# Optimization experiments

Measured on AMD Instinct MI355X. Metric: run time of the kernel, lower is better.

## Reference

```python
import jax, jax.numpy as jnp
import numpy as np

B, C_IN, N_NODES = 128, 64, 1024
N_TRIPLES = 3 * (N_NODES - 1)  # node 0 is the shared zero vector


def _btc(x, idx, w, b):
    # x: [B, C, N]; idx: [B, 3M]; w: [O, C, 3]; b: [O]
    Bv, C, _ = x.shape
    T = idx.shape[1]
    g = jnp.take_along_axis(x, jnp.broadcast_to(idx[:, None, :], (Bv, C, T)), axis=2)
    g = g.reshape(Bv, C, T // 3, 3)  # stride-3 kernel-3 conv == per-triple contraction
    out = jnp.einsum('bcnk,ock->bon', g, w) + b[None, :, None]
    zero = jnp.zeros((Bv, out.shape[1], 1), dtype=out.dtype)
    return jnp.concatenate([zero, out], axis=2)  # re-prepend zero node -> [B, O, N]


def _tln(x):
    mean = jnp.mean(x, axis=(1, 2), keepdims=True)
    std = jnp.std(x, axis=(1, 2), ddof=1, keepdims=True)  # torch.std is unbiased
    return (x - mean) / (std + 1e-5)


def _tower(x, idx, p):
    x = jax.nn.leaky_relu(_tln(_btc(x, idx, p['w_conv1'], p['b_conv1'])), 0.01)
    x = jax.nn.leaky_relu(_tln(_btc(x, idx, p['w_conv2'], p['b_conv2'])), 0.01)
    x = _tln(_btc(x, idx, p['w_conv3'], p['b_conv3']))
    x = jnp.max(x, axis=2)  # DynamicPooling -> [B, 64]
    x = jax.nn.leaky_relu(x @ p['w_fc1'].T + p['b_fc1'], 0.01)
    return x @ p['w_fc2'].T + p['b_fc2']  # [B, 1]  (Dropout is identity at eval)


def setup_inputs() -> dict:
    key = jax.random.key(0)
    ks = jax.random.split(key, 12)
    s = 0.05
    return {
        'data1': jax.random.normal(ks[0], (B, C_IN, N_NODES), jnp.float32),
        'idx1': jax.random.randint(ks[1], (B, N_TRIPLES, 1), 0, N_NODES, dtype=jnp.int64)
                if jax.config.jax_enable_x64 else
                jax.random.randint(ks[1], (B, N_TRIPLES, 1), 0, N_NODES).astype(jnp.int32),
        'data2': jax.random.normal(ks[2], (B, C_IN, N_NODES), jnp.float32),
        'idx2': jax.random.randint(ks[3], (B, N_TRIPLES, 1), 0, N_NODES).astype(jnp.int32),
        'w_conv1': jax.random.normal(ks[4], (256, C_IN, 3), jnp.float32) * s,
        'b_conv1': jnp.zeros((256,), jnp.float32),
        'w_conv2': jax.random.normal(ks[5], (128, 256, 3), jnp.float32) * s,
        'b_conv2': jnp.zeros((128,), jnp.float32),
        'w_conv3': jax.random.normal(ks[6], (64, 128, 3), jnp.float32) * s,
        'b_conv3': jnp.zeros((64,), jnp.float32),
        'w_fc1': jax.random.normal(ks[7], (32, 64), jnp.float32) * s,
        'b_fc1': jnp.zeros((32,), jnp.float32),
        'w_fc2': jax.random.normal(ks[8], (1, 32), jnp.float32) * s,
        'b_fc2': jnp.zeros((1,), jnp.float32),
    }


def reference(data1, idx1, data2, idx2,
              w_conv1, b_conv1, w_conv2, b_conv2, w_conv3, b_conv3,
              w_fc1, b_fc1, w_fc2, b_fc2):
    p = dict(w_conv1=w_conv1, b_conv1=b_conv1, w_conv2=w_conv2, b_conv2=b_conv2,
             w_conv3=w_conv3, b_conv3=b_conv3, w_fc1=w_fc1, b_fc1=b_fc1,
             w_fc2=w_fc2, b_fc2=b_fc2)
    y1 = _tower(data1, idx1[..., 0], p)
    y2 = _tower(data2, idx2[..., 0], p)
    return jnp.squeeze(jax.nn.sigmoid(y1 - y2), axis=1)  # [B]
```

## Files before the change

### kernel.cpp

```cpp
#include <hip/hip_runtime.h>
#include <math.h>

typedef __attribute__((ext_vector_type(8))) short short8;
typedef __attribute__((ext_vector_type(4))) float f32x4;
typedef __attribute__((ext_vector_type(2))) float f32x2;

#define LRELU(x) ((x) > 0.0f ? (x) : 0.01f * (x))

__device__ __forceinline__ float bf2f(unsigned short h) {
    return __uint_as_float(((unsigned int)h) << 16);
}
__device__ __forceinline__ unsigned short f2bf(float f) {
    unsigned int u = __float_as_uint(f);
    return (unsigned short)((u + 0x7FFFu + ((u >> 16) & 1u)) >> 16);
}
__device__ __forceinline__ unsigned int pack_bf16_pair(float lo, float hi) {
    unsigned int ul = __float_as_uint(lo) + 0x8000u;
    unsigned int uh = __float_as_uint(hi) + 0x8000u;
    return (ul >> 16) | (uh & 0xFFFF0000u);
}
__device__ __forceinline__ float2 stats_from(const float* sums, int b, float count) {
    float s = sums[2 * b], q = sums[2 * b + 1];
    float mean = s / count;
    float var = (q - s * s / count) / (count - 1.0f);
    var = fmaxf(var, 0.0f);
    return make_float2(mean, 1.0f / (sqrtf(var) + 1e-5f));
}
__device__ __forceinline__ void atomicMaxF(float* a, float v) {
    if (v >= 0.0f) atomicMax((int*)a, __float_as_int(v));
    else           atomicMin((unsigned int*)a, __float_as_uint(v));
}
__device__ __forceinline__ unsigned int norm_pair(unsigned int u, float a, float c) {
    f32x2 v;
    v.x = __uint_as_float(u << 16);
    v.y = __uint_as_float(u & 0xFFFF0000u);
    v = v * a + c;
    f32x2 m = v * 0.01f;
    v = __builtin_elementwise_max(v, m);
    return pack_bf16_pair(v.x, v.y);
}
__device__ __forceinline__ uint4 norm8(uint4 v, float a, float c) {
    v.x = norm_pair(v.x, a, c); v.y = norm_pair(v.y, a, c);
    v.z = norm_pair(v.z, a, c); v.w = norm_pair(v.w, a, c);
    return v;
}
__device__ __forceinline__ unsigned int fp8x4_nact(unsigned int u, float a, float c) {
    f32x2 lo = __builtin_amdgcn_cvt_pk_f32_fp8(u, false);
    f32x2 hi = __builtin_amdgcn_cvt_pk_f32_fp8(u, true);
    lo = lo * a + c; hi = hi * a + c;
    f32x2 ml = lo * 0.01f, mh = hi * 0.01f;
    lo = __builtin_elementwise_max(lo, ml);
    hi = __builtin_elementwise_max(hi, mh);
    int r = __builtin_amdgcn_cvt_pk_fp8_f32(lo.x, lo.y, 0, false);
    r = __builtin_amdgcn_cvt_pk_fp8_f32(hi.x, hi.y, r, true);
    return (unsigned int)r;
}

template <int MT, int WM>
__device__ __forceinline__ void mfma_step(const unsigned short* wt, const unsigned short* gt,
                                          f32x4 (&acc)[MT][4],
                                          int wo, int wn, int quad, int l15, int blkid)
{
#pragma unroll
    for (int st = 0; st < 2; ++st) {
        short8 af[MT], bfv[4];
        const int qb = st * 4 + quad;
#pragma unroll
        for (int i = 0; i < MT; i++) {
            const int orow = wo * WM + i * 16 + l15;
            af[i] = *(const short8*)&wt[orow * 64 + ((qb ^ blkid) << 3)];
        }
#pragma unroll
        for (int t = 0; t < 4; t++) {
            const int nrow = wn * 64 + t * 16 + l15;
            bfv[t] = *(const short8*)&gt[nrow * 64 + ((qb ^ blkid) << 3)];
        }
#pragma unroll
        for (int i = 0; i < MT; i++)
#pragma unroll
            for (int t = 0; t < 4; t++)
                acc[i][t] = __builtin_amdgcn_mfma_f32_16x16x32_bf16(
                    af[i], bfv[t], acc[i][t], 0, 0, 0);
    }
}

__global__ void prep_weights(const float* __restrict__ w, unsigned short* __restrict__ wq,
                             int O, int Cin)
{
    const int K = 3 * Cin, total = O * K;
    for (int i = blockIdx.x * blockDim.x + threadIdx.x; i < total;
         i += gridDim.x * blockDim.x) {
        int o = i / K, kp = i - o * K;
        int j = kp / Cin, c = kp - j * Cin;
        wq[i] = f2bf(w[(o * Cin + c) * 3 + j]);
    }
}

__global__ void prep_weights_fp8(const float* __restrict__ w, unsigned char* __restrict__ wq,
                                 int O, int Cin)
{
    const int K = 3 * Cin, total = (O * K) >> 2;
    for (int i = blockIdx.x * blockDim.x + threadIdx.x; i < total;
         i += gridDim.x * blockDim.x) {
        const int e0 = i << 2;
        const int o = e0 / K, kp0 = e0 - o * K;
        float f0, f1, f2, f3;
        {
            int kp = kp0 + 0, j = kp / Cin, c = kp - j * Cin; f0 = w[(o * Cin + c) * 3 + j];
        }
        {
            int kp = kp0 + 1, j = kp / Cin, c = kp - j * Cin; f1 = w[(o * Cin + c) * 3 + j];
        }
        {
            int kp = kp0 + 2, j = kp / Cin, c = kp - j * Cin; f2 = w[(o * Cin + c) * 3 + j];
        }
        {
            int kp = kp0 + 3, j = kp / Cin, c = kp - j * Cin; f3 = w[(o * Cin + c) * 3 + j];
        }
        int r = __builtin_amdgcn_cvt_pk_fp8_f32(f0, f1, 0, false);
        r = __builtin_amdgcn_cvt_pk_fp8_f32(f2, f3, r, true);
        *(unsigned int*)&wq[e0] = (unsigned int)r;
    }
}

__global__ __launch_bounds__(256) void transpose_in(const float* __restrict__ inA,
                                                    const float* __restrict__ inB,
                                                    unsigned short* __restrict__ xT)
{
    const int b = blockIdx.y, n0 = blockIdx.x * 64;
    const float* in = (b >= 128 ? inB : inA) + ((size_t)(b & 127) * 64) * 1024;
    const int tid = threadIdx.x;
    __shared__ float tile[64][65];
    const int nn = tid & 63, cw = tid >> 6;
#pragma unroll
    for (int i = 0; i < 16; i++) {
        int c = i * 4 + cw;
        tile[c][nn] = in[(size_t)c * 1024 + n0 + nn];
    }
    __syncthreads();
    const int n = tid >> 2, cp = (tid & 3) * 16;
    unsigned int pk[8];
#pragma unroll
    for (int i = 0; i < 8; i++) {
        unsigned short lo = f2bf(tile[cp + 2 * i][n]);
        unsigned short hi = f2bf(tile[cp + 2 * i + 1][n]);
        pk[i] = (unsigned int)lo | ((unsigned int)hi << 16);
    }
    unsigned short* dst = xT + ((size_t)b * 1024 + n0 + n) * 64 + cp;
    uint4 v0 = {pk[0], pk[1], pk[2], pk[3]};
    uint4 v1 = {pk[4], pk[5], pk[6], pk[7]};
    *(uint4*)dst = v0;
    *(uint4*)(dst + 8) = v1;
}

__global__ __launch_bounds__(256) void norm_act_fp8(unsigned char* __restrict__ a,
                                                    const float* __restrict__ sums,
                                                    float count)
{
    const int b = blockIdx.y;
    float2 st = stats_from(sums, b, count);
    const float na = st.y, nc = -st.x * st.y;
    uint4* p = (uint4*)(a + ((size_t)b << 18));
    const int base = blockIdx.x * 256 + threadIdx.x;
#pragma unroll
    for (int it = 0; it < 4; ++it) {
        const int idx = base + it * 4096;
        uint4 v = p[idx];
        v.x = fp8x4_nact(v.x, na, nc);
        v.y = fp8x4_nact(v.y, na, nc);
        v.z = fp8x4_nact(v.z, na, nc);
        v.w = fp8x4_nact(v.w, na, nc);
        p[idx] = v;
    }
}

template <int BM, bool POOL, bool NORM, bool FP8IN, bool FP8OUT>
__global__ __launch_bounds__(256, 2) void conv_mfma(
    const void* __restrict__ xTv,
    const int* __restrict__ idxA,
    const int* __restrict__ idxB,
    const unsigned short* __restrict__ wq,
    const float* __restrict__ bias,
    void* __restrict__ out,
    float* __restrict__ sums,
    float* __restrict__ pmax,
    const float* __restrict__ normSums,
    float normCount, int Cin, int cinShift, int O, int K)
{
    constexpr int WM = BM / 2, MT = WM / 16;
    constexpr int NW = (BM == 128) ? 4 : 2;
    const int b   = blockIdx.x;
    const int o0  = blockIdx.y * BM;
    const int nt0 = blockIdx.z << 7;
    const int tid = threadIdx.x;
    const int lane = tid & 63, wave = tid >> 6;
    const int wo = wave & 1, wn = wave >> 1;
    const int quad = lane >> 4, l15 = lane & 15;
    const int blkid = lane & 7;

    __shared__ __align__(16) unsigned short wt[BM * 64];
    __shared__ __align__(16) unsigned short gt[128 * 64];

    f32x4 acc[MT][4];
#pragma unroll
    for (int i = 0; i < MT; i++)
#pragma unroll
        for (int t = 0; t < 4; t++) acc[i][t] = (f32x4){0.f, 0.f, 0.f, 0.f};

    const unsigned short* xTb16 = (const unsigned short*)xTv + (((size_t)b) << 10) * (size_t)Cin;
    const unsigned char*  xTb8  = (const unsigned char*)xTv  + (((size_t)b) << 10) * (size_t)Cin;
    const int* idxb = (b >= 128 ? idxB : idxA) + (size_t)(b & 127) * 3069;

    float na = 1.0f, nc = 0.0f;
    if (NORM) {
        float2 st = stats_from(normSums, b, normCount);
        na = st.y; nc = -st.x * st.y;
    }

    const int gr = tid >> 1, gh = tid & 1;
    int s0, s1, s2;
    {
        int n = nt0 + gr;
        int t0 = (n == 0) ? 0 : (n - 1);
        s0 = idxb[3 * t0]; s1 = idxb[3 * t0 + 1]; s2 = idxb[3 * t0 + 2];
    }
    const int wr   = (BM == 128) ? (tid >> 1) : (tid >> 2);
    const int wseg = (BM == 128) ? (tid & 1) : (tid & 3);
    const unsigned short* wrow = wq + (size_t)(o0 + wr) * K + wseg * (NW * 8);
    const int gswz = gr & 7, wswz = wr & 7;

    uint4 g0A, g1A, g2A, g3A, w0A, w1A, w2A, w3A;
    uint4 g0B, g1B, g2B, g3B, w0B, w1B, w2B, w3B;

#define LOADC(S, KC) {                                                           \
        const int k64_ = (KC) << 6;                                              \
        const int j_   = k64_ >> cinShift;                                       \
        const int c0_  = k64_ & (Cin - 1);                                       \
        const int src_ = (j_ == 0) ? s0 : ((j_ == 1) ? s1 : s2);                 \
        if (FP8IN) {                                                             \
            const uint4* gp_ = (const uint4*)(xTb8 + (size_t)src_ * Cin + c0_ + gh * 32); \
            g0##S = gp_[0]; g1##S = gp_[1];                                      \
        } else {                                                                 \
            const uint4* gp_ = (const uint4*)(xTb16 + (size_t)src_ * Cin + c0_ + gh * 32); \
            g0##S = gp_[0]; g1##S = gp_[1]; g2##S = gp_[2]; g3##S = gp_[3];      \
        }                                                                        \
        const uint4* wp_ = (const uint4*)(wrow + k64_);                          \
        w0##S = wp_[0]; w1##S = wp_[1];                                          \
        if (NW == 4) { w2##S = wp_[2]; w3##S = wp_[3]; }                         \
    }

#define STAGE(S) {                                                               \
        uint4 h0, h1, h2, h3;                                                    \
        h0 = g0##S; h1 = g1##S; h2 = g2##S; h3 = g3##S;                          \
        if (NORM) {                                                              \
            h0 = norm8(h0, na, nc); h1 = norm8(h1, na, nc);                      \
            h2 = norm8(h2, na, nc); h3 = norm8(h3, na, nc);                      \
        }                                                                        \
        *(uint4*)&gt[gr * 64 + (((gh << 2) | 0) ^ gswz) * 8] = h0;               \
        *(uint4*)&gt[gr * 64 + (((gh << 2) | 1) ^ gswz) * 8] = h1;               \
        *(uint4*)&gt[gr * 64 + (((gh << 2) | 2) ^ gswz) * 8] = h2;               \
        *(uint4*)&gt[gr * 64 + (((gh << 2) | 3) ^ gswz) * 8] = h3;               \
        *(uint4*)&wt[wr * 64 + ((wseg * NW + 0) ^ wswz) * 8] = w0##S;            \
        *(uint4*)&wt[wr * 64 + ((wseg * NW + 1) ^ wswz) * 8] = w1##S;            \
        if (NW == 4) {                                                           \
            *(uint4*)&wt[wr * 64 + ((wseg * NW + 2) ^ wswz) * 8] = w2##S;        \
            *(uint4*)&wt[wr * 64 + ((wseg * NW + 3) ^ wswz) * 8] = w3##S;        \
        }                                                                        \
    }

    const int nChunks = K >> 6;
    LOADC(A, 0);
    if (nChunks > 1) LOADC(B, 1);
    int kc = 0;
    for (; kc + 2 <= nChunks; kc += 2) {
        if (kc) __syncthreads();
        STAGE(A);
        if (kc + 2 < nChunks) LOADC(A, kc + 2);
        __syncthreads();
        mfma_step<MT, WM>(wt, gt, acc, wo, wn, quad, l15, blkid);
        __syncthreads();
        STAGE(B);
        if (kc + 3 < nChunks) LOADC(B, kc + 3);
        __syncthreads();
        mfma_step<MT, WM>(wt, gt, acc, wo, wn, quad, l15, blkid);
    }
    if (kc < nChunks) {
        __syncthreads();
        STAGE(A);
        __syncthreads();
        mfma_step<MT, WM>(wt, gt, acc, wo, wn, quad, l15, blkid);
    }
#undef LOADC
#undef STAGE

    float lsum = 0.f, lsq = 0.f;
#pragma unroll
    for (int i = 0; i < MT; i++) {
        const int ob = o0 + wo * WM + i * 16 + quad * 4;
        const float4 bv = *(const float4*)(bias + ob);
        float mx0 = -1e30f, mx1 = -1e30f, mx2 = -1e30f, mx3 = -1e30f;
#pragma unroll
        for (int t = 0; t < 4; t++) {
            const int n = nt0 + wn * 64 + t * 16 + l15;
            float v0 = acc[i][t][0] + bv.x;
            float v1 = acc[i][t][1] + bv.y;
            float v2 = acc[i][t][2] + bv.z;
            float v3 = acc[i][t][3] + bv.w;
            if (n == 0) { v0 = v1 = v2 = v3 = 0.f; }
            lsum += v0 + v1 + v2 + v3;
            lsq  += v0 * v0 + v1 * v1 + v2 * v2 + v3 * v3;
            if (POOL) {
                mx0 = fmaxf(mx0, v0); mx1 = fmaxf(mx1, v1);
                mx2 = fmaxf(mx2, v2); mx3 = fmaxf(mx3, v3);
            } else if (FP8OUT) {
                int r = __builtin_amdgcn_cvt_pk_fp8_f32(v0, v1, 0, false);
                r = __builtin_amdgcn_cvt_pk_fp8_f32(v2, v3, r, true);
                *(unsigned int*)&((unsigned char*)out)[((size_t)b * 1024 + n) * O + ob] =
                    (unsigned int)r;
            } else {
                uint2 pk;
                pk.x = pack_bf16_pair(v0, v1);
                pk.y = pack_bf16_pair(v2, v3);
                *(uint2*)&((unsigned short*)out)[((size_t)b * 1024 + n) * O + ob] = pk;
            }
        }
        if (POOL) {
#pragma unroll
            for (int off = 1; off < 16; off <<= 1) {
                mx0 = fmaxf(mx0, __shfl_xor(mx0, off));
                mx1 = fmaxf(mx1, __shfl_xor(mx1, off));
                mx2 = fmaxf(mx2, __shfl_xor(mx2, off));
                mx3 = fmaxf(mx3, __shfl_xor(mx3, off));
            }
            if (l15 == 0) {
                atomicMaxF(&pmax[(size_t)b * 64 + ob + 0], mx0);
                atomicMaxF(&pmax[(size_t)b * 64 + ob + 1], mx1);
                atomicMaxF(&pmax[(size_t)b * 64 + ob + 2], mx2);
                atomicMaxF(&pmax[(size_t)b * 64 + ob + 3], mx3);
            }
        }
    }
#pragma unroll
    for (int off = 32; off > 0; off >>= 1) {
        lsum += __shfl_down(lsum, off);
        lsq  += __shfl_down(lsq, off);
    }
    float* red = (float*)wt;
    if (lane == 0) { red[wave] = lsum; red[4 + wave] = lsq; }
    __syncthreads();
    if (tid == 0) {
        atomicAdd(&sums[2 * b + 0], red[0] + red[1] + red[2] + red[3]);
        atomicAdd(&sums[2 * b + 1], red[4] + red[5] + red[6] + red[7]);
    }
}

__global__ __launch_bounds__(256, 2) void conv2_fp8(
    const unsigned char* __restrict__ a1,
    const int* __restrict__ idxA,
    const int* __restrict__ idxB,
    const unsigned char* __restrict__ wq8,
    const float* __restrict__ bias,
    unsigned short* __restrict__ out,
    float* __restrict__ sums)
{
    const int b   = blockIdx.x;
    const int nt0 = blockIdx.z << 7;
    const int tid = threadIdx.x;
    const int lane = tid & 63, wave = tid >> 6;
    const int wo = wave & 1, wn = wave >> 1;
    const int quad = lane >> 4, l15 = lane & 15;
    const int blkid = lane & 7;

    __shared__ __align__(16) unsigned char wt8[128 * 128];
    __shared__ __align__(16) unsigned char gt8[128 * 128];

    f32x4 acc[4][4];
#pragma unroll
    for (int i = 0; i < 4; i++)
#pragma unroll
        for (int t = 0; t < 4; t++) acc[i][t] = (f32x4){0.f, 0.f, 0.f, 0.f};

    const unsigned char* xb = a1 + (((size_t)b) << 10) * 256;
    const int* idxb = (b >= 128 ? idxB : idxA) + (size_t)(b & 127) * 3069;

    const int gr = tid >> 1, gh = tid & 1;
    int si0, si1, si2;
    {
        int n = nt0 + gr;
        int t0 = (n == 0) ? 0 : (n - 1);
        si0 = idxb[3 * t0]; si1 = idxb[3 * t0 + 1]; si2 = idxb[3 * t0 + 2];
    }
    const unsigned char* wrow = wq8 + (size_t)gr * 768 + gh * 64;
    const int swz = gr & 7;

    uint4 g0A, g1A, g2A, g3A, w0A, w1A, w2A, w3A;
    uint4 g0B, g1B, g2B, g3B, w0B, w1B, w2B, w3B;

#define LOADC2(S, KC) {                                                          \
        const int j_  = (KC) >> 1;                                               \
        const int c0_ = ((KC) & 1) << 7;                                         \
        const int src_ = (j_ == 0) ? si0 : ((j_ == 1) ? si1 : si2);              \
        const uint4* gp_ = (const uint4*)(xb + (size_t)src_ * 256 + c0_ + gh * 64); \
        g0##S = gp_[0]; g1##S = gp_[1]; g2##S = gp_[2]; g3##S = gp_[3];          \
        const uint4* wp_ = (const uint4*)(wrow + (KC) * 128);                    \
        w0##S = wp_[0]; w1##S = wp_[1]; w2##S = wp_[2]; w3##S = wp_[3];          \
    }

#define STAGE2(S) {                                                              \
        *(uint4*)&gt8[gr * 128 + (((gh << 2) | 0) ^ swz) * 16] = g0##S;          \
        *(uint4*)&gt8[gr * 128 + (((gh << 2) | 1) ^ swz) * 16] = g1##S;          \
        *(uint4*)&gt8[gr * 128 + (((gh << 2) | 2) ^ swz) * 16] = g2##S;          \
        *(uint4*)&gt8[gr * 128 + (((gh << 2) | 3) ^ swz) * 16] = g3##S;          \
        *(uint4*)&wt8[gr * 128 + (((gh << 2) | 0) ^ swz) * 16] = w0##S;          \
        *(uint4*)&wt8[gr * 128 + (((gh << 2) | 1) ^ swz) * 16] = w1##S;          \
        *(uint4*)&wt8[gr * 128 + (((gh << 2) | 2) ^ swz) * 16] = w2##S;          \
        *(uint4*)&wt8[gr * 128 + (((gh << 2) | 3) ^ swz) * 16] = w3##S;          \
    }

#define MFMA_STEP2 {                                                             \
        _Pragma("unroll")                                                        \
        for (int st = 0; st < 4; ++st) {                                         \
            long af0, af1, af2, af3, bf0, bf1, bf2, bf3;                         \
            const int qb = st * 4 + quad;                                        \
            const int cg = qb >> 1, ch = (qb & 1) << 3;                          \
            {                                                                    \
                const int r0 = wo * 64 + 0 * 16 + l15;                           \
                af0 = *(const long*)&wt8[r0 * 128 + ((cg ^ blkid) << 4) + ch];   \
                const int r1 = wo * 64 + 1 * 16 + l15;                           \
                af1 = *(const long*)&wt8[r1 * 128 + ((cg ^ blkid) << 4) + ch];   \
                const int r2 = wo * 64 + 2 * 16 + l15;                           \
                af2 = *(const long*)&wt8[r2 * 128 + ((cg ^ blkid) << 4) + ch];   \
                const int r3 = wo * 64 + 3 * 16 + l15;                           \
                af3 = *(const long*)&wt8[r3 * 128 + ((cg ^ blkid) << 4) + ch];   \
                const int n0 = wn * 64 + 0 * 16 + l15;                           \
                bf0 = *(const long*)&gt8[n0 * 128 + ((cg ^ blkid) << 4) + ch];   \
                const int n1 = wn * 64 + 1 * 16 + l15;                           \
                bf1 = *(const long*)&gt8[n1 * 128 + ((cg ^ blkid) << 4) + ch];   \
                const int n2 = wn * 64 + 2 * 16 + l15;                           \
                bf2 = *(const long*)&gt8[n2 * 128 + ((cg ^ blkid) << 4) + ch];   \
                const int n3 = wn * 64 + 3 * 16 + l15;                           \
                bf3 = *(const long*)&gt8[n3 * 128 + ((cg ^ blkid) << 4) + ch];   \
            }                                                                    \
            acc[0][0] = __builtin_amdgcn_mfma_f32_16x16x32_fp8_fp8(af0, bf0, acc[0][0], 0, 0, 0); \
            acc[0][1] = __builtin_amdgcn_mfma_f32_16x16x32_fp8_fp8(af0, bf1, acc[0][1], 0, 0, 0); \
            acc[0][2] = __builtin_amdgcn_mfma_f32_16x16x32_fp8_fp8(af0, bf2, acc[0][2], 0, 0, 0); \
            acc[0][3] = __builtin_amdgcn_mfma_f32_16x16x32_fp8_fp8(af0, bf3, acc[0][3], 0, 0, 0); \
            acc[1][0] = __builtin_amdgcn_mfma_f32_16x16x32_fp8_fp8(af1, bf0, acc[1][0], 0, 0, 0); \
            acc[1][1] = __builtin_amdgcn_mfma_f32_16x16x32_fp8_fp8(af1, bf1, acc[1][1], 0, 0, 0); \
            acc[1][2] = __builtin_amdgcn_mfma_f32_16x16x32_fp8_fp8(af1, bf2, acc[1][2], 0, 0, 0); \
            acc[1][3] = __builtin_amdgcn_mfma_f32_16x16x32_fp8_fp8(af1, bf3, acc[1][3], 0, 0, 0); \
            acc[2][0] = __builtin_amdgcn_mfma_f32_16x16x32_fp8_fp8(af2, bf0, acc[2][0], 0, 0, 0); \
            acc[2][1] = __builtin_amdgcn_mfma_f32_16x16x32_fp8_fp8(af2, bf1, acc[2][1], 0, 0, 0); \
            acc[2][2] = __builtin_amdgcn_mfma_f32_16x16x32_fp8_fp8(af2, bf2, acc[2][2], 0, 0, 0); \
            acc[2][3] = __builtin_amdgcn_mfma_f32_16x16x32_fp8_fp8(af2, bf3, acc[2][3], 0, 0, 0); \
            acc[3][0] = __builtin_amdgcn_mfma_f32_16x16x32_fp8_fp8(af3, bf0, acc[3][0], 0, 0, 0); \
            acc[3][1] = __builtin_amdgcn_mfma_f32_16x16x32_fp8_fp8(af3, bf1, acc[3][1], 0, 0, 0); \
            acc[3][2] = __builtin_amdgcn_mfma_f32_16x16x32_fp8_fp8(af3, bf2, acc[3][2], 0, 0, 0); \
            acc[3][3] = __builtin_amdgcn_mfma_f32_16x16x32_fp8_fp8(af3, bf3, acc[3][3], 0, 0, 0); \
        }                                                                        \
    }

    LOADC2(A, 0);
    LOADC2(B, 1);
    int kc = 0;
    for (; kc + 2 <= 6; kc += 2) {
        if (kc) __syncthreads();
        STAGE2(A);
        if (kc + 2 < 6) LOADC2(A, kc + 2);
        __syncthreads();
        MFMA_STEP2;
        __syncthreads();
        STAGE2(B);
        if (kc + 3 < 6) LOADC2(B, kc + 3);
        __syncthreads();
        MFMA_STEP2;
    }
#undef LOADC2
#undef STAGE2
#undef MFMA_STEP2

    float lsum = 0.f, lsq = 0.f;
#pragma unroll
    for (int i = 0; i < 4; i++) {
        const int ob = wo * 64 + i * 16 + quad * 4;
        const float4 bv = *(const float4*)(bias + ob);
#pragma unroll
        for (int t = 0; t < 4; t++) {
            const int n = nt0 + wn * 64 + t * 16 + l15;
            float v0 = acc[i][t][0] + bv.x;
            float v1 = acc[i][t][1] + bv.y;
            float v2 = acc[i][t][2] + bv.z;
            float v3 = acc[i][t][3] + bv.w;
            if (n == 0) { v0 = v1 = v2 = v3 = 0.f; }
            lsum += v0 + v1 + v2 + v3;
            lsq  += v0 * v0 + v1 * v1 + v2 * v2 + v3 * v3;
            uint2 pk;
            pk.x = pack_bf16_pair(v0, v1);
            pk.y = pack_bf16_pair(v2, v3);
            *(uint2*)&out[((size_t)b * 1024 + n) * 128 + ob] = pk;
        }
    }
#pragma unroll
    for (int off = 32; off > 0; off >>= 1) {
        lsum += __shfl_down(lsum, off);
        lsq  += __shfl_down(lsq, off);
    }
    float* red = (float*)wt8;
    if (lane == 0) { red[wave] = lsum; red[4 + wave] = lsq; }
    __syncthreads();
    if (tid == 0) {
        atomicAdd(&sums[2 * b + 0], red[0] + red[1] + red[2] + red[3]);
        atomicAdd(&sums[2 * b + 1], red[4] + red[5] + red[6] + red[7]);
    }
}

__global__ __launch_bounds__(64) void fc_head(
    const float* __restrict__ pmax, const float* __restrict__ sums3, float count,
    const float* __restrict__ w_fc1, const float* __restrict__ b_fc1,
    const float* __restrict__ w_fc2, const float* __restrict__ b_fc2,
    float* __restrict__ y)
{
    const int b = blockIdx.x, t = threadIdx.x;
    __shared__ float pooled[64];
    __shared__ float hid[32];
    float2 s = stats_from(sums3, b, count);
    pooled[t] = (pmax[(size_t)b * 64 + t] - s.x) * s.y;
    __syncthreads();
    if (t < 32) {
        float h = b_fc1[t];
#pragma unroll
        for (int c = 0; c < 64; c++) h += pooled[c] * w_fc1[t * 64 + c];
        hid[t] = LRELU(h);
    }
    __syncthreads();
    if (t == 0) {
        float v = b_fc2[0];
#pragma unroll
        for (int c = 0; c < 32; c++) v += hid[c] * w_fc2[c];
        y[b] = v;
    }
}

__global__ void sigmoid_diff(const float* __restrict__ y1,
                             const float* __restrict__ y2,
                             float* __restrict__ out)
{
    int b = threadIdx.x;
    if (b < 128) out[b] = 1.0f / (1.0f + expf(-(y1[b] - y2[b])));
}

extern "C" void kernel_launch(void* const* d_in, const int* in_sizes, int n_in,
                              void* d_out, int out_size, void* d_ws, size_t ws_size,
                              hipStream_t stream)
{
    const float* data1 = (const float*)d_in[0];
    const int*   idx1  = (const int*)d_in[1];
    const float* data2 = (const float*)d_in[2];
    const int*   idx2  = (const int*)d_in[3];
    const float* w1 = (const float*)d_in[4];
    const float* b1 = (const float*)d_in[5];
    const float* w2 = (const float*)d_in[6];
    const float* b2 = (const float*)d_in[7];
    const float* w3 = (const float*)d_in[8];
    const float* b3 = (const float*)d_in[9];
    const float* wfc1 = (const float*)d_in[10];
    const float* bfc1 = (const float*)d_in[11];
    const float* wfc2 = (const float*)d_in[12];
    const float* bfc2 = (const float*)d_in[13];

    const size_t needM = (size_t)256 * 1024 * (64 * 2 + 256 * 1 + 128 * 2) + 768 * 1024;
    const bool merged = ws_size >= needM;
    const int nB = merged ? 256 : 128;
    const size_t szXT = (size_t)nB * 1024 * 64 * 2;
    const size_t szA1 = (size_t)nB * 1024 * 256;
    const size_t szA2 = (size_t)nB * 1024 * 128 * 2;

    char* ws = (char*)d_ws;
    unsigned short* xT = (unsigned short*)ws;
    unsigned char*  a1 = (unsigned char*)(ws + szXT);
    unsigned short* a2 = (unsigned short*)(ws + szXT + szA1);
    char* tail = ws + szXT + szA1 + szA2;
    unsigned short* wq1 = (unsigned short*)tail;
    unsigned char*  wq2f8 = (unsigned char*)(tail + 128 * 1024);
    unsigned short* wq3 = (unsigned short*)(tail + 384 * 1024);
    float* sums = (float*)(tail + 448 * 1024);
    float* pmax = (float*)(tail + 512 * 1024);
    float* yv   = (float*)(tail + 640 * 1024);

    prep_weights<<<96, 256, 0, stream>>>(w1, wq1, 256, 64);
    prep_weights_fp8<<<96, 256, 0, stream>>>(w2, wq2f8, 128, 256);
    prep_weights<<<96, 256, 0, stream>>>(w3, wq3, 64, 128);

    const int nIter = merged ? 1 : 2;
    for (int t = 0; t < nIter; ++t) {
        const float* dA = (merged || t == 0) ? data1 : data2;
        const float* dB = merged ? data2 : dA;
        const int* iA = (merged || t == 0) ? idx1 : idx2;
        const int* iB = merged ? idx2 : iA;
        float* s1 = sums;
        float* s2 = sums + nB * 2;
        float* s3 = sums + nB * 4;

        hipMemsetAsync(sums, 0, 3 * (size_t)nB * 2 * sizeof(float), stream);
        hipMemsetAsync(pmax, 0xFF, (size_t)nB * 64 * sizeof(float), stream);

        transpose_in<<<dim3(16, nB), 256, 0, stream>>>(dA, dB, xT);

        conv_mfma<128, false, false, false, true><<<dim3(nB, 2, 8), 256, 0, stream>>>(
            xT, iA, iB, wq1, b1, a1, s1, nullptr, nullptr, 0.0f, 64, 6, 256, 192);

        norm_act_fp8<<<dim3(16, nB), 256, 0, stream>>>(a1, s1, 256.0f * 1024.0f);

        conv2_fp8<<<dim3(nB, 1, 8), 256, 0, stream>>>(
            a1, iA, iB, wq2f8, b2, a2, s2);

        conv_mfma<64, true, true, false, false><<<dim3(nB, 1, 8), 256, 0, stream>>>(
            a2, iA, iB, wq3, b3, nullptr, s3, pmax, s2, 128.0f * 1024.0f, 128, 7, 64, 384);

        fc_head<<<nB, 64, 0, stream>>>(pmax, s3, 64.0f * 1024.0f,
                                       wfc1, bfc1, wfc2, bfc2,
                                       yv + (merged ? 0 : t * 128));
    }
    sigmoid_diff<<<1, 128, 0, stream>>>(yv, yv + 128, (float*)d_out);
}
```

Baseline: 324.1 us.

## Merge weight prep launches, fold memsets into transpose, defer weight loads

Folds the three weight-conversion kernels into a single prep_all launch and moves the zeroing of sums and pmax into the first block of transpose_in, which drops two memset calls and two kernel launches. In both conv kernels the weight tile load moves from the prefetch into the staging step, which frees eight uint4 registers per thread. The freed registers are used to raise the launch bounds minimum-blocks hint from 2 to 3 for higher occupancy. The trade-off is that weight global loads are no longer overlapped with the previous MFMA step, and a tighter register budget could cause spills.

```diff
diff --git a/kernel.cpp b/kernel.cpp
--- a/kernel.cpp
+++ b/kernel.cpp
@@ -84,52 +84,48 @@
     }
 }
 
-__global__ void prep_weights(const float* __restrict__ w, unsigned short* __restrict__ wq,
-                             int O, int Cin)
-{
-    const int K = 3 * Cin, total = O * K;
-    for (int i = blockIdx.x * blockDim.x + threadIdx.x; i < total;
-         i += gridDim.x * blockDim.x) {
-        int o = i / K, kp = i - o * K;
-        int j = kp / Cin, c = kp - j * Cin;
-        wq[i] = f2bf(w[(o * Cin + c) * 3 + j]);
-    }
-}
-
-__global__ void prep_weights_fp8(const float* __restrict__ w, unsigned char* __restrict__ wq,
-                                 int O, int Cin)
-{
-    const int K = 3 * Cin, total = (O * K) >> 2;
-    for (int i = blockIdx.x * blockDim.x + threadIdx.x; i < total;
-         i += gridDim.x * blockDim.x) {
+__global__ void prep_all(const float* __restrict__ w1, unsigned short* __restrict__ wq1,
+                         const float* __restrict__ w2, unsigned char* __restrict__ wq2,
+                         const float* __restrict__ w3, unsigned short* __restrict__ wq3)
+{
+    const int tid = blockIdx.x * blockDim.x + threadIdx.x;
+    const int stride = gridDim.x * blockDim.x;
+    for (int i = tid; i < 256 * 192; i += stride) {
+        int o = i / 192, kp = i - o * 192;
+        int j = kp >> 6, c = kp & 63;
+        wq1[i] = f2bf(w1[(o * 64 + c) * 3 + j]);
+    }
+    for (int i = tid; i < (128 * 768) >> 2; i += stride) {
         const int e0 = i << 2;
-        const int o = e0 / K, kp0 = e0 - o * K;
-        float f0, f1, f2, f3;
-        {
-            int kp = kp0 + 0, j = kp / Cin, c = kp - j * Cin; f0 = w[(o * Cin + c) * 3 + j];
-        }
-        {
-            int kp = kp0 + 1, j = kp / Cin, c = kp - j * Cin; f1 = w[(o * Cin + c) * 3 + j];
-        }
-        {
-            int kp = kp0 + 2, j = kp / Cin, c = kp - j * Cin; f2 = w[(o * Cin + c) * 3 + j];
-        }
-        {
-            int kp = kp0 + 3, j = kp / Cin, c = kp - j * Cin; f3 = w[(o * Cin + c) * 3 + j];
-        }
+        const int o = e0 / 768, kp0 = e0 - o * 768;
+        const int j = kp0 >> 8, c0 = kp0 & 255;
+        const float* src = &w2[(o * 256 + c0) * 3 + j];
+        float f0 = src[0], f1 = src[3], f2 = src[6], f3 = src[9];
         int r = __builtin_amdgcn_cvt_pk_fp8_f32(f0, f1, 0, false);
         r = __builtin_amdgcn_cvt_pk_fp8_f32(f2, f3, r, true);
-        *(unsigned int*)&wq[e0] = (unsigned int)r;
+        *(unsigned int*)&wq2[e0] = (unsigned int)r;
+    }
+    for (int i = tid; i < 64 * 384; i += stride) {
+        int o = i / 384, kp = i - o * 384;
+        int j = kp >> 7, c = kp & 127;
+        wq3[i] = f2bf(w3[(o * 128 + c) * 3 + j]);
     }
 }
 
 __global__ __launch_bounds__(256) void transpose_in(const float* __restrict__ inA,
                                                     const float* __restrict__ inB,
-                                                    unsigned short* __restrict__ xT)
+                                                    unsigned short* __restrict__ xT,
+                                                    float* __restrict__ sums,
+                                                    unsigned int* __restrict__ pmax)
 {
     const int b = blockIdx.y, n0 = blockIdx.x * 64;
     const float* in = (b >= 128 ? inB : inA) + ((size_t)(b & 127) * 64) * 1024;
     const int tid = threadIdx.x;
+    if (blockIdx.x == 0 && blockIdx.y == 0) {
+        const int nBv = gridDim.y;
+        for (int i = tid; i < 3 * nBv * 2; i += 256) sums[i] = 0.0f;
+        for (int i = tid; i < nBv * 64; i += 256) pmax[i] = 0xFFFFFFFFu;
+    }
     __shared__ float tile[64][65];
     const int nn = tid & 63, cw = tid >> 6;
 #pragma unroll
@@ -175,7 +171,7 @@
 }
 
 template <int BM, bool POOL, bool NORM, bool FP8IN, bool FP8OUT>
-__global__ __launch_bounds__(256, 2) void conv_mfma(
+__global__ __launch_bounds__(256, 3) void conv_mfma(
     const void* __restrict__ xTv,
     const int* __restrict__ idxA,
     const int* __restrict__ idxB,
@@ -229,8 +225,8 @@
     const unsigned short* wrow = wq + (size_t)(o0 + wr) * K + wseg * (NW * 8);
     const int gswz = gr & 7, wswz = wr & 7;
 
-    uint4 g0A, g1A, g2A, g3A, w0A, w1A, w2A, w3A;
-    uint4 g0B, g1B, g2B, g3B, w0B, w1B, w2B, w3B;
+    uint4 g0A, g1A, g2A, g3A;
+    uint4 g0B, g1B, g2B, g3B;
 
 #define LOADC(S, KC) {                                                           \
         const int k64_ = (KC) << 6;                                              \
@@ -244,12 +240,12 @@
             const uint4* gp_ = (const uint4*)(xTb16 + (size_t)src_ * Cin + c0_ + gh * 32); \
             g0##S = gp_[0]; g1##S = gp_[1]; g2##S = gp_[2]; g3##S = gp_[3];      \
         }                                                                        \
-        const uint4* wp_ = (const uint4*)(wrow + k64_);                          \
-        w0##S = wp_[0]; w1##S = wp_[1];                                          \
-        if (NW == 4) { w2##S = wp_[2]; w3##S = wp_[3]; }                         \
-    }
-
-#define STAGE(S) {                                                               \
+    }
+
+#define STAGE(S, KC) {                                                           \
+        const uint4* wp_ = (const uint4*)(wrow + ((KC) << 6));                   \
+        uint4 wv0 = wp_[0], wv1 = wp_[1], wv2, wv3;                              \
+        if (NW == 4) { wv2 = wp_[2]; wv3 = wp_[3]; }                             \
         uint4 h0, h1, h2, h3;                                                    \
         h0 = g0##S; h1 = g1##S; h2 = g2##S; h3 = g3##S;                          \
         if (NORM) {                                                              \
@@ -260,11 +256,11 @@
         *(uint4*)&gt[gr * 64 + (((gh << 2) | 1) ^ gswz) * 8] = h1;               \
         *(uint4*)&gt[gr * 64 + (((gh << 2) | 2) ^ gswz) * 8] = h2;               \
         *(uint4*)&gt[gr * 64 + (((gh << 2) | 3) ^ gswz) * 8] = h3;               \
-        *(uint4*)&wt[wr * 64 + ((wseg * NW + 0) ^ wswz) * 8] = w0##S;            \
-        *(uint4*)&wt[wr * 64 + ((wseg * NW + 1) ^ wswz) * 8] = w1##S;            \
+        *(uint4*)&wt[wr * 64 + ((wseg * NW + 0) ^ wswz) * 8] = wv0;              \
+        *(uint4*)&wt[wr * 64 + ((wseg * NW + 1) ^ wswz) * 8] = wv1;              \
         if (NW == 4) {                                                           \
-            *(uint4*)&wt[wr * 64 + ((wseg * NW + 2) ^ wswz) * 8] = w2##S;        \
-            *(uint4*)&wt[wr * 64 + ((wseg * NW + 3) ^ wswz) * 8] = w3##S;        \
+            *(uint4*)&wt[wr * 64 + ((wseg * NW + 2) ^ wswz) * 8] = wv2;          \
+            *(uint4*)&wt[wr * 64 + ((wseg * NW + 3) ^ wswz) * 8] = wv3;          \
         }                                                                        \
     }
 
@@ -274,19 +270,19 @@
     int kc = 0;
     for (; kc + 2 <= nChunks; kc += 2) {
         if (kc) __syncthreads();
-        STAGE(A);
+        STAGE(A, kc);
         if (kc + 2 < nChunks) LOADC(A, kc + 2);
         __syncthreads();
         mfma_step<MT, WM>(wt, gt, acc, wo, wn, quad, l15, blkid);
         __syncthreads();
-        STAGE(B);
+        STAGE(B, kc + 1);
         if (kc + 3 < nChunks) LOADC(B, kc + 3);
         __syncthreads();
         mfma_step<MT, WM>(wt, gt, acc, wo, wn, quad, l15, blkid);
     }
     if (kc < nChunks) {
         __syncthreads();
-        STAGE(A);
+        STAGE(A, kc);
         __syncthreads();
         mfma_step<MT, WM>(wt, gt, acc, wo, wn, quad, l15, blkid);
     }
@@ -354,7 +350,7 @@
     }
 }
 
-__global__ __launch_bounds__(256, 2) void conv2_fp8(
+__global__ __launch_bounds__(256, 3) void conv2_fp8(
     const unsigned char* __restrict__ a1,
     const int* __restrict__ idxA,
     const int* __restrict__ idxB,
@@ -393,8 +389,8 @@
     const unsigned char* wrow = wq8 + (size_t)gr * 768 + gh * 64;
     const int swz = gr & 7;
 
-    uint4 g0A, g1A, g2A, g3A, w0A, w1A, w2A, w3A;
-    uint4 g0B, g1B, g2B, g3B, w0B, w1B, w2B, w3B;
+    uint4 g0A, g1A, g2A, g3A;
+    uint4 g0B, g1B, g2B, g3B;
 
 #define LOADC2(S, KC) {                                                          \
         const int j_  = (KC) >> 1;                                               \
@@ -402,19 +398,19 @@
         const int src_ = (j_ == 0) ? si0 : ((j_ == 1) ? si1 : si2);              \
         const uint4* gp_ = (const uint4*)(xb + (size_t)src_ * 256 + c0_ + gh * 64); \
         g0##S = gp_[0]; g1##S = gp_[1]; g2##S = gp_[2]; g3##S = gp_[3];          \
+    }
+
+#define STAGE2(S, KC) {                                                          \
         const uint4* wp_ = (const uint4*)(wrow + (KC) * 128);                    \
-        w0##S = wp_[0]; w1##S = wp_[1]; w2##S = wp_[2]; w3##S = wp_[3];          \
-    }
-
-#define STAGE2(S) {                                                              \
+        uint4 wv0 = wp_[0], wv1 = wp_[1], wv2 = wp_[2], wv3 = wp_[3];            \
         *(uint4*)&gt8[gr * 128 + (((gh << 2) | 0) ^ swz) * 16] = g0##S;          \
         *(uint4*)&gt8[gr * 128 + (((gh << 2) | 1) ^ swz) * 16] = g1##S;          \
         *(uint4*)&gt8[gr * 128 + (((gh << 2) | 2) ^ swz) * 16] = g2##S;          \
         *(uint4*)&gt8[gr * 128 + (((gh << 2) | 3) ^ swz) * 16] = g3##S;          \
-        *(uint4*)&wt8[gr * 128 + (((gh << 2) | 0) ^ swz) * 16] = w0##S;          \
-        *(uint4*)&wt8[gr * 128 + (((gh << 2) | 1) ^ swz) * 16] = w1##S;          \
-        *(uint4*)&wt8[gr * 128 + (((gh << 2) | 2) ^ swz) * 16] = w2##S;          \
-        *(uint4*)&wt8[gr * 128 + (((gh << 2) | 3) ^ swz) * 16] = w3##S;          \
+        *(uint4*)&wt8[gr * 128 + (((gh << 2) | 0) ^ swz) * 16] = wv0;            \
+        *(uint4*)&wt8[gr * 128 + (((gh << 2) | 1) ^ swz) * 16] = wv1;            \
+        *(uint4*)&wt8[gr * 128 + (((gh << 2) | 2) ^ swz) * 16] = wv2;            \
+        *(uint4*)&wt8[gr * 128 + (((gh << 2) | 3) ^ swz) * 16] = wv3;            \
     }
 
 #define MFMA_STEP2 {                                                             \
@@ -465,12 +461,12 @@
     int kc = 0;
     for (; kc + 2 <= 6; kc += 2) {
         if (kc) __syncthreads();
-        STAGE2(A);
+        STAGE2(A, kc);
         if (kc + 2 < 6) LOADC2(A, kc + 2);
         __syncthreads();
         MFMA_STEP2;
         __syncthreads();
-        STAGE2(B);
+        STAGE2(B, kc + 1);
         if (kc + 3 < 6) LOADC2(B, kc + 3);
         __syncthreads();
         MFMA_STEP2;
@@ -587,9 +583,7 @@
     float* pmax = (float*)(tail + 512 * 1024);
     float* yv   = (float*)(tail + 640 * 1024);
 
-    prep_weights<<<96, 256, 0, stream>>>(w1, wq1, 256, 64);
-    prep_weights_fp8<<<96, 256, 0, stream>>>(w2, wq2f8, 128, 256);
-    prep_weights<<<96, 256, 0, stream>>>(w3, wq3, 64, 128);
+    prep_all<<<96, 256, 0, stream>>>(w1, wq1, w2, wq2f8, w3, wq3);
 
     const int nIter = merged ? 1 : 2;
     for (int t = 0; t < nIter; ++t) {
@@ -601,10 +595,8 @@
         float* s2 = sums + nB * 2;
         float* s3 = sums + nB * 4;
 
-        hipMemsetAsync(sums, 0, 3 * (size_t)nB * 2 * sizeof(float), stream);
-        hipMemsetAsync(pmax, 0xFF, (size_t)nB * 64 * sizeof(float), stream);
-
-        transpose_in<<<dim3(16, nB), 256, 0, stream>>>(dA, dB, xT);
+        transpose_in<<<dim3(16, nB), 256, 0, stream>>>(dA, dB, xT, sums,
+                                                       (unsigned int*)pmax);
 
         conv_mfma<128, false, false, false, true><<<dim3(nB, 2, 8), 256, 0, stream>>>(
             xT, iA, iB, wq1, b1, a1, s1, nullptr, nullptr, 0.0f, 64, 6, 256, 192);
```

Measured after the change: 318.1 us. About the same (-1.8%).
